# Kernel optimization log

Measured on AMD Instinct MI355X. Metric: run time of the kernel, lower is better.

Reference implementation:

```python
import jax, jax.numpy as jnp
import numpy as np

VOCAB = 100000
DIM = 300
SEQ = 200
BATCH = 1024


def setup_inputs() -> dict:
    key = jax.random.key(0)
    ks = jax.random.split(key, 7)
    tokens = jax.random.randint(ks[0], (SEQ, BATCH), 0, VOCAB, dtype=jnp.int32)
    static_lut = jax.random.normal(ks[1], (VOCAB, DIM), dtype=jnp.float32)
    # lut = pretrained vectors + N(0, 0.01) noise
    lut = static_lut + 0.01 * jax.random.normal(ks[2], (VOCAB, DIM), dtype=jnp.float32)
    W1 = jax.random.normal(ks[3], (600, 600), dtype=jnp.float32) / np.sqrt(600.0)
    b1 = jnp.zeros((600,), dtype=jnp.float32)
    W2 = jax.random.normal(ks[4], (1, 600), dtype=jnp.float32) / np.sqrt(600.0)
    b2 = jnp.zeros((1,), dtype=jnp.float32)
    return {"tokens": tokens, "lut": lut, "static_lut": static_lut,
            "W1": W1, "b1": b1, "W2": W2, "b2": b2}


def _first_occurrence_mask(tokens):
    # tokens: [S, B]. mask[i, b] = 1 iff tokens[i, b] is the first occurrence
    # of that token value in column b (emulates per-column set() dedup).
    S = tokens.shape[0]
    eq = tokens[:, None, :] == tokens[None, :, :]          # [S, S, B]
    first_idx = jnp.argmax(eq, axis=1)                      # [S, B] first j with same token
    return (first_idx == jnp.arange(S, dtype=first_idx.dtype)[:, None])


def reference(tokens, lut, static_lut, W1, b1, W2, b2):
    mask = _first_occurrence_mask(tokens).astype(lut.dtype)  # [S, B]
    # dedup embedding-bag sums over unique tokens per column
    e_learn = jnp.einsum('sbd,sb->bd', lut[tokens], mask)          # [B, 300]
    e_static = jnp.einsum('sbd,sb->bd', static_lut[tokens], mask)  # [B, 300]
    hidden = jnp.concatenate([e_learn, e_static], axis=-1)         # [B, 600]
    h = jax.nn.relu(hidden @ W1.T + b1)                            # [B, 600]
    out = h @ W2.T + b2                                            # [B, 1]
    return out[:, 0]                                               # [B]
```

## Files before the change

kernel.cpp:

```cpp
#include <hip/hip_runtime.h>
#include <limits.h>

#define SEQ   200
#define BATCH 1024
#define DIM   300
#define HID   600
#define VOCAB 100000

#define NQ    4
#define NBKT  64

#define BW    4
#define JCH   12
#define JPER  (HID / JCH)

#define HIDDEN_ELEMS (BATCH * HID)
#define HIDDEN_BYTES ((size_t)HIDDEN_ELEMS * 4)

#define SORT_BYTES  ((size_t)BATCH * 256 * 4)
#define OFF_NK      SORT_BYTES
#define OFF_HID4    (SORT_BYTES + 65536)
#define OFF_HIDDEN  (OFF_HID4 + 4 * HIDDEN_BYTES)

__global__ __launch_bounds__(256) void sort_kernel(
    const int* __restrict__ tokens,
    int* __restrict__ sorted_g,
    int* __restrict__ nk_g) {
  const int b    = blockIdx.x;
  const int tid  = threadIdx.x;
  const int w    = tid >> 6;
  const int lane = tid & 63;

  __shared__ int hist[NBKT];
  __shared__ int base[NBKT];
  __shared__ int cur[NBKT];
  __shared__ int stok[SEQ];
  __shared__ int keepf[SEQ];
  __shared__ int wsum[4];

  if (tid < NBKT) { hist[tid] = 0; cur[tid] = 0; }
  __syncthreads();

  int t = 0, bk = 0;
  if (tid < SEQ) {
    t  = tokens[tid * BATCH + b];
    bk = (int)((unsigned)t * (unsigned)NBKT / (unsigned)VOCAB);
    atomicAdd(&hist[bk], 1);
  }
  __syncthreads();

  if (tid < NBKT) {
    const int v = hist[tid];
    int incl = v;
#pragma unroll
    for (int off = 1; off < NBKT; off <<= 1) {
      const int n = __shfl_up(incl, off, 64);
      if (lane >= off) incl += n;
    }
    base[tid] = incl - v;
  }
  __syncthreads();

  int pos = -1;
  if (tid < SEQ) {
    pos = base[bk] + atomicAdd(&cur[bk], 1);
    stok[pos] = t;
  }
  __syncthreads();

  if (tid < SEQ) {
    int kf = 1;
    const int b0 = base[bk];
    for (int j = b0; j < pos; ++j) {
      if (stok[j] == t) { kf = 0; break; }
    }
    keepf[pos] = kf;
  }
  __syncthreads();

  const int val = (tid < SEQ) ? keepf[tid] : 0;
  int incl = val;
#pragma unroll
  for (int off = 1; off < 64; off <<= 1) {
    const int n = __shfl_up(incl, off, 64);
    if (lane >= off) incl += n;
  }
  if (lane == 63) wsum[w] = incl;
  __syncthreads();

  int prefix = 0;
  for (int q = 0; q < w; ++q) prefix += wsum[q];
  if (tid < SEQ && val) sorted_g[b * 256 + prefix + incl - val] = stok[tid];
  if (tid == 0) nk_g[b] = wsum[0] + wsum[1] + wsum[2] + wsum[3];
}

__global__ __launch_bounds__(192) void embed_gather_kernel(
    const int* __restrict__ sorted_g,
    const int* __restrict__ nk_g,
    const float* __restrict__ lut,
    const float* __restrict__ slut,
    float* __restrict__ hid4) {
  const int b   = blockIdx.x;
  const int q   = blockIdx.y;
  const int tid = threadIdx.x;

  const int nk = nk_g[b];
  const int i0 = (q * nk) / NQ;
  const int i1 = ((q + 1) * nk) / NQ;

  const int tab_i = tid / 75;
  const int slot  = tid % 75;
  if (tab_i < 2) {
    const float* __restrict__ tab = tab_i ? slut : lut;
    const int* __restrict__ rows = sorted_g + b * 256;
    float4 a = make_float4(0.f, 0.f, 0.f, 0.f);
#pragma unroll 16
    for (int i = i0; i < i1; ++i) {
      const float4 v = ((const float4*)(tab + (size_t)rows[i] * DIM))[slot];
      a.x += v.x; a.y += v.y; a.z += v.z; a.w += v.w;
    }
    float* dst = hid4 + ((size_t)q * BATCH + b) * HID + tab_i * DIM;
    ((float4*)dst)[slot] = a;
  }
}

__global__ __launch_bounds__(256) void combine_kernel(
    const float* __restrict__ hid4, float* __restrict__ hidden) {
  const int i = blockIdx.x * 256 + threadIdx.x;
  const int n4 = HIDDEN_ELEMS / 4;
  if (i < n4) {
    const float4* p = (const float4*)hid4;
    const float4 a = p[i];
    const float4 b = p[i + n4];
    const float4 c = p[i + 2 * n4];
    const float4 d = p[i + 3 * n4];
    float4 s;
    s.x = (a.x + b.x) + (c.x + d.x);
    s.y = (a.y + b.y) + (c.y + d.y);
    s.z = (a.z + b.z) + (c.z + d.z);
    s.w = (a.w + b.w) + (c.w + d.w);
    ((float4*)hidden)[i] = s;
  }
}

__global__ __launch_bounds__(256) void out_init_kernel(
    float* __restrict__ out, const float* __restrict__ b2) {
  const int i = blockIdx.x * 256 + threadIdx.x;
  if (i < BATCH) out[i] = b2[0];
}

template <int CTRL>
__device__ __forceinline__ float dpp_add(float x) {
  const int y = __builtin_amdgcn_update_dpp(
      0, __float_as_int(x), CTRL, 0xf, 0xf, true);
  return x + __int_as_float(y);
}

__device__ __forceinline__ float wave_sum(float h) {
  h = dpp_add<0x111>(h);
  h = dpp_add<0x112>(h);
  h = dpp_add<0x114>(h);
  h = dpp_add<0x118>(h);
  h = dpp_add<0x142>(h);
  h = dpp_add<0x143>(h);
  return h;
}

__global__ __launch_bounds__(256) void mlp_kernel(
    const float* __restrict__ hidden,
    const float* __restrict__ W1,
    const float* __restrict__ b1,
    const float* __restrict__ W2,
    float* __restrict__ out) {
  const int wave = threadIdx.x >> 6;
  const int lane = threadIdx.x & 63;
  const int b0   = (blockIdx.x * 4 + wave) * BW;
  const int j0   = blockIdx.y * JPER;

  float a[BW][10];
#pragma unroll
  for (int bb = 0; bb < BW; ++bb) {
    const float* __restrict__ hb = hidden + (size_t)(b0 + bb) * HID;
#pragma unroll
    for (int i = 0; i < 9; ++i) a[bb][i] = hb[lane + 64 * i];
    a[bb][9] = (lane < 24) ? hb[lane + 576] : 0.f;
  }

  float acc[BW] = {0.f, 0.f, 0.f, 0.f};

#pragma unroll 2
  for (int jj = 0; jj < JPER; ++jj) {
    const int j = j0 + jj;
    const float* __restrict__ wr = W1 + (size_t)j * HID;
    float d0 = 0.f, d1 = 0.f, d2 = 0.f, d3 = 0.f;
#pragma unroll
    for (int i = 0; i < 9; ++i) {
      const float w = wr[lane + 64 * i];
      d0 += a[0][i] * w;
      d1 += a[1][i] * w;
      d2 += a[2][i] * w;
      d3 += a[3][i] * w;
    }
    {
      const float w = (lane < 24) ? wr[lane + 576] : 0.f;
      d0 += a[0][9] * w;
      d1 += a[1][9] * w;
      d2 += a[2][9] * w;
      d3 += a[3][9] * w;
    }
    d0 = wave_sum(d0); d1 = wave_sum(d1);
    d2 = wave_sum(d2); d3 = wave_sum(d3);
    const float b1j = b1[j];
    const float w2j = W2[j];
    acc[0] += fmaxf(d0 + b1j, 0.f) * w2j;
    acc[1] += fmaxf(d1 + b1j, 0.f) * w2j;
    acc[2] += fmaxf(d2 + b1j, 0.f) * w2j;
    acc[3] += fmaxf(d3 + b1j, 0.f) * w2j;
  }

  if (lane == 63) {
#pragma unroll
    for (int bb = 0; bb < BW; ++bb) atomicAdd(&out[b0 + bb], acc[bb]);
  }
}

extern "C" void kernel_launch(void* const* d_in, const int* in_sizes, int n_in,
                              void* d_out, int out_size, void* d_ws, size_t ws_size,
                              hipStream_t stream) {
  const int*   tokens = (const int*)  d_in[0];
  const float* lut    = (const float*)d_in[1];
  const float* slut   = (const float*)d_in[2];
  const float* W1     = (const float*)d_in[3];
  const float* b1     = (const float*)d_in[4];
  const float* W2     = (const float*)d_in[5];
  const float* b2     = (const float*)d_in[6];
  float* out = (float*)d_out;

  int*   sorted_g = (int*)d_ws;
  int*   nk_g     = (int*)((char*)d_ws + OFF_NK);
  float* hid4     = (float*)((char*)d_ws + OFF_HID4);
  float* hidden   = (float*)((char*)d_ws + OFF_HIDDEN);

  out_init_kernel<<<(BATCH + 255) / 256, 256, 0, stream>>>(out, b2);
  sort_kernel<<<BATCH, 256, 0, stream>>>(tokens, sorted_g, nk_g);
  embed_gather_kernel<<<dim3(BATCH, NQ), 192, 0, stream>>>(
      sorted_g, nk_g, lut, slut, hid4);
  combine_kernel<<<(HIDDEN_ELEMS / 4 + 255) / 256, 256, 0, stream>>>(
      hid4, hidden);
  mlp_kernel<<<dim3(BATCH / (4 * BW), JCH), 256, 0, stream>>>(
      hidden, W1, b1, W2, out);
}
```

Baseline: 118.6 us.

## Fuse partial-sum combine into MLP load and widen batch tile per wave

Removes the separate combine kernel: the MLP kernel now sums the four partial embedding buffers while loading its activations, which saves a launch and a full write-and-read of the hidden matrix. Each wave also handles 8 batch rows instead of 4, so every W1 load is reused across more rows. The gather loop unroll drops from 16 to 8. The wider tile doubles register use for activations and halves the number of MLP blocks, which may lower occupancy and parallelism. Each MLP block column also re-reads the four partial buffers, giving more redundant reads across the 12 j-chunks.

```diff
diff --git a/kernel.cpp b/kernel.cpp
--- a/kernel.cpp
+++ b/kernel.cpp
@@ -10,7 +10,7 @@
 #define NQ    4
 #define NBKT  64
 
-#define BW    4
+#define BW    8
 #define JCH   12
 #define JPER  (HID / JCH)
 
@@ -20,7 +20,6 @@
 #define SORT_BYTES  ((size_t)BATCH * 256 * 4)
 #define OFF_NK      SORT_BYTES
 #define OFF_HID4    (SORT_BYTES + 65536)
-#define OFF_HIDDEN  (OFF_HID4 + 4 * HIDDEN_BYTES)
 
 __global__ __launch_bounds__(256) void sort_kernel(
     const int* __restrict__ tokens,
@@ -114,32 +113,13 @@
     const float* __restrict__ tab = tab_i ? slut : lut;
     const int* __restrict__ rows = sorted_g + b * 256;
     float4 a = make_float4(0.f, 0.f, 0.f, 0.f);
-#pragma unroll 16
+#pragma unroll 8
     for (int i = i0; i < i1; ++i) {
       const float4 v = ((const float4*)(tab + (size_t)rows[i] * DIM))[slot];
       a.x += v.x; a.y += v.y; a.z += v.z; a.w += v.w;
     }
     float* dst = hid4 + ((size_t)q * BATCH + b) * HID + tab_i * DIM;
     ((float4*)dst)[slot] = a;
-  }
-}
-
-__global__ __launch_bounds__(256) void combine_kernel(
-    const float* __restrict__ hid4, float* __restrict__ hidden) {
-  const int i = blockIdx.x * 256 + threadIdx.x;
-  const int n4 = HIDDEN_ELEMS / 4;
-  if (i < n4) {
-    const float4* p = (const float4*)hid4;
-    const float4 a = p[i];
-    const float4 b = p[i + n4];
-    const float4 c = p[i + 2 * n4];
-    const float4 d = p[i + 3 * n4];
-    float4 s;
-    s.x = (a.x + b.x) + (c.x + d.x);
-    s.y = (a.y + b.y) + (c.y + d.y);
-    s.z = (a.z + b.z) + (c.z + d.z);
-    s.w = (a.w + b.w) + (c.w + d.w);
-    ((float4*)hidden)[i] = s;
   }
 }
 
@@ -167,7 +147,7 @@
 }
 
 __global__ __launch_bounds__(256) void mlp_kernel(
-    const float* __restrict__ hidden,
+    const float* __restrict__ hid4,
     const float* __restrict__ W1,
     const float* __restrict__ b1,
     const float* __restrict__ W2,
@@ -176,46 +156,50 @@
   const int lane = threadIdx.x & 63;
   const int b0   = (blockIdx.x * 4 + wave) * BW;
   const int j0   = blockIdx.y * JPER;
+  const size_t P = (size_t)BATCH * HID;
 
   float a[BW][10];
 #pragma unroll
   for (int bb = 0; bb < BW; ++bb) {
-    const float* __restrict__ hb = hidden + (size_t)(b0 + bb) * HID;
-#pragma unroll
-    for (int i = 0; i < 9; ++i) a[bb][i] = hb[lane + 64 * i];
-    a[bb][9] = (lane < 24) ? hb[lane + 576] : 0.f;
-  }
-
-  float acc[BW] = {0.f, 0.f, 0.f, 0.f};
+    const float* __restrict__ hb = hid4 + (size_t)(b0 + bb) * HID;
+#pragma unroll
+    for (int i = 0; i < 9; ++i) {
+      const int k = lane + 64 * i;
+      a[bb][i] = (hb[k] + hb[k + P]) + (hb[k + 2 * P] + hb[k + 3 * P]);
+    }
+    if (lane < 24) {
+      const int k = lane + 576;
+      a[bb][9] = (hb[k] + hb[k + P]) + (hb[k + 2 * P] + hb[k + 3 * P]);
+    } else {
+      a[bb][9] = 0.f;
+    }
+  }
+
+  float acc[BW] = {0.f, 0.f, 0.f, 0.f, 0.f, 0.f, 0.f, 0.f};
 
 #pragma unroll 2
   for (int jj = 0; jj < JPER; ++jj) {
     const int j = j0 + jj;
     const float* __restrict__ wr = W1 + (size_t)j * HID;
-    float d0 = 0.f, d1 = 0.f, d2 = 0.f, d3 = 0.f;
+    float d[BW] = {0.f, 0.f, 0.f, 0.f, 0.f, 0.f, 0.f, 0.f};
 #pragma unroll
     for (int i = 0; i < 9; ++i) {
       const float w = wr[lane + 64 * i];
-      d0 += a[0][i] * w;
-      d1 += a[1][i] * w;
-      d2 += a[2][i] * w;
-      d3 += a[3][i] * w;
+#pragma unroll
+      for (int bb = 0; bb < BW; ++bb) d[bb] += a[bb][i] * w;
     }
     {
       const float w = (lane < 24) ? wr[lane + 576] : 0.f;
-      d0 += a[0][9] * w;
-      d1 += a[1][9] * w;
-      d2 += a[2][9] * w;
-      d3 += a[3][9] * w;
-    }
-    d0 = wave_sum(d0); d1 = wave_sum(d1);
-    d2 = wave_sum(d2); d3 = wave_sum(d3);
+#pragma unroll
+      for (int bb = 0; bb < BW; ++bb) d[bb] += a[bb][9] * w;
+    }
+#pragma unroll
+    for (int bb = 0; bb < BW; ++bb) d[bb] = wave_sum(d[bb]);
     const float b1j = b1[j];
     const float w2j = W2[j];
-    acc[0] += fmaxf(d0 + b1j, 0.f) * w2j;
-    acc[1] += fmaxf(d1 + b1j, 0.f) * w2j;
-    acc[2] += fmaxf(d2 + b1j, 0.f) * w2j;
-    acc[3] += fmaxf(d3 + b1j, 0.f) * w2j;
+#pragma unroll
+    for (int bb = 0; bb < BW; ++bb)
+      acc[bb] += fmaxf(d[bb] + b1j, 0.f) * w2j;
   }
 
   if (lane == 63) {
@@ -239,14 +223,11 @@
   int*   sorted_g = (int*)d_ws;
   int*   nk_g     = (int*)((char*)d_ws + OFF_NK);
   float* hid4     = (float*)((char*)d_ws + OFF_HID4);
-  float* hidden   = (float*)((char*)d_ws + OFF_HIDDEN);
 
   out_init_kernel<<<(BATCH + 255) / 256, 256, 0, stream>>>(out, b2);
   sort_kernel<<<BATCH, 256, 0, stream>>>(tokens, sorted_g, nk_g);
   embed_gather_kernel<<<dim3(BATCH, NQ), 192, 0, stream>>>(
       sorted_g, nk_g, lut, slut, hid4);
-  combine_kernel<<<(HIDDEN_ELEMS / 4 + 255) / 256, 256, 0, stream>>>(
-      hid4, hidden);
   mlp_kernel<<<dim3(BATCH / (4 * BW), JCH), 256, 0, stream>>>(
-      hidden, W1, b1, W2, out);
-}
+      hid4, W1, b1, W2, out);
+}
```

Result: slower. 152.1 us (+28.2%).
